# Kernel tuning notes

Hardware: AMD Instinct MI355X
Metric: run time of the kernel (lower is better)

## Reference

```python
import jax, jax.numpy as jnp
import numpy as np

SOM_H, SOM_W = 16, 16
K = SOM_H * SOM_W          # num_embeddings = 256
EMB_D = 32                 # embedding_dim
ALPHA, BETA = 6.0, 1.0


def _build_tables():
    """Static SOM grid neighbor tables (rectangular geometry).
    ind[k] is a 0/1 row over the K codebook entries marking k and its
    up/down/left/right grid neighbors; counts[k] = number of neighbors incl self.
    Replaces the original per-voxel Python loop with a constant lookup table.
    """
    ind = np.zeros((K, K), np.float32)
    for idx in range(K):
        h, w = divmod(idx, SOM_W)
        neigh = [idx]
        if h - 1 >= 0:
            neigh.append((h - 1) * SOM_W + w)
        if h + 1 < SOM_H:
            neigh.append((h + 1) * SOM_W + w)
        if w - 1 >= 0:
            neigh.append(h * SOM_W + (w - 1))
        if w + 1 < SOM_W:
            neigh.append(h * SOM_W + (w + 1))
        ind[idx, neigh] = 1.0
    counts = ind.sum(axis=1)
    return jnp.asarray(ind), jnp.asarray(counts)

_IND_TABLE, _COUNTS = _build_tables()


def setup_inputs() -> dict:
    key = jax.random.key(0)
    k1, k2 = jax.random.split(key)
    x = jax.random.normal(k1, (8, EMB_D, 32, 32, 32), dtype=jnp.float32)  # [B,C,D,H,W]
    W = jax.random.normal(k2, (K, EMB_D), dtype=jnp.float32)              # codebook
    return {"x": x, "W": W}


def reference(x, W):
    # channels-last: [B, D, H, Wd, C]
    inputs = jnp.transpose(x, (0, 2, 3, 4, 1))
    in_shape = inputs.shape
    flat = inputs.reshape(-1, EMB_D)                    # [N, d]
    flat_sg = jax.lax.stop_gradient(flat)               # matches flat_inputs.detach()

    # squared Euclidean distances to all codebook entries: [N, K]
    dist = (jnp.sum(flat_sg ** 2, axis=1, keepdims=True)
            + jnp.sum(W ** 2, axis=1)
            - 2.0 * flat_sg @ W.T)

    enc_idx = jnp.argmin(dist, axis=1)                  # [N]
    encodings = jax.nn.one_hot(enc_idx, K, dtype=inputs.dtype)  # [N, K]

    quantized = (encodings @ W).reshape(in_shape)
    commitment_loss = jnp.mean((quantized - inputs) ** 2)

    # vectorized neighbor indicator + counts via static table gather
    indicator = _IND_TABLE[enc_idx]                     # [N, K], constant wrt floats
    total_neighbors = jnp.sum(_COUNTS[enc_idx])
    somloss = jnp.sum(dist * indicator) / total_neighbors

    loss = ALPHA * commitment_loss + BETA * somloss

    # straight-through estimator
    quantized_st = inputs + jax.lax.stop_gradient(quantized - inputs)
    out = jnp.transpose(quantized_st, (0, 4, 1, 2, 3))  # back to [B,C,D,H,W]
    return loss, out, encodings
```

## Files before the change

### kernel.cpp

```cpp
#include <hip/hip_runtime.h>


#define SOM_K      256
#define EMB_D      32
#define WPAD       36
#define N_VOX      262144
#define SPATIAL    32768
#define OUT_ELEMS  8388608
#define COMMIT_DEN 8388608.0f
#define NSLOT      256

#define CONST_AS __attribute__((address_space(4)))

__global__ __launch_bounds__(256) void som_prep_kernel(float* __restrict__ ws) {
  float4* p = (float4*)ws;
  int t = threadIdx.x;
#pragma unroll
  for (int i = 0; i < 4; ++i) p[i * 256 + t] = make_float4(0.f, 0.f, 0.f, 0.f);
}

__global__ __launch_bounds__(256) void som_main_kernel(
    const float* __restrict__ x,
    const float* __restrict__ w,
    float* __restrict__ slots,
    float* __restrict__ out,
    float* __restrict__ enc) {
  __shared__ __align__(16) float wl[SOM_K * WPAD];
  __shared__ float wsql[SOM_K];

  const int t = threadIdx.x;
  const CONST_AS float* wc = (const CONST_AS float*)(unsigned long long)w;

  const int n    = blockIdx.x * 256 + t;
  const int base = (n >> 15) * (EMB_D * SPATIAL) + (n & (SPATIAL - 1));
  float xv[EMB_D];
#pragma unroll
  for (int c = 0; c < EMB_D; ++c) xv[c] = x[base + c * SPATIAL];

#pragma unroll
  for (int i = 0; i < 32; ++i) {
    int e = i * 256 + t;
    int r = e >> 5, c = e & 31;
    wl[r * WPAD + c] = w[e];
  }
  {
    float s = 0.0f;
#pragma unroll
    for (int c = 0; c < EMB_D; ++c) {
      float v = w[t * EMB_D + c];
      s = fmaf(v, v, s);
    }
    wsql[t] = s;
  }
  __syncthreads();

  float xsq = 0.0f;
#pragma unroll
  for (int c = 0; c < EMB_D; ++c) xsq = fmaf(xv[c], xv[c], xsq);

  float best = 3.402823466e38f;
  int   bidx = 0;
#pragma unroll 2
  for (int k = 0; k < SOM_K; ++k) {
    const CONST_AS float* wr = wc + (k << 5);
    float dot = 0.0f;
#pragma unroll
    for (int j = 0; j < EMB_D; ++j) dot = fmaf(wr[j], xv[j], dot);
    float d = (xsq + wsql[k]) - 2.0f * dot;
    if (d < best) { best = d; bidx = k; }
  }

  {
    const int lane = t & 63, wave = t >> 6;
    float* ep = enc + (size_t)(blockIdx.x * 256 + wave * 64) * SOM_K + lane;
    const int c1 = lane + 64, c2 = lane + 128, c3 = lane + 192;
    for (int row = 0; row < 64; ++row) {
      const int src = __builtin_amdgcn_readlane(bidx, row);
      ep[0]   = (lane == src) ? 1.0f : 0.0f;
      ep[64]  = (c1   == src) ? 1.0f : 0.0f;
      ep[128] = (c2   == src) ? 1.0f : 0.0f;
      ep[192] = (c3   == src) ? 1.0f : 0.0f;
      ep += SOM_K;
    }
  }

  float commit = 0.0f;
  {
    const float4* qrow = (const float4*)(wl + bidx * WPAD);
#pragma unroll
    for (int j = 0; j < 8; ++j) {
      float4 q = qrow[j];
      float qq[4] = { q.x, q.y, q.z, q.w };
#pragma unroll
      for (int u = 0; u < 4; ++u) {
        int c = 4 * j + u;
        out[base + c * SPATIAL] = qq[u];
        float df = qq[u] - xv[c];
        commit = fmaf(df, df, commit);
      }
    }
  }

  float som = best;
  float cnt = 1.0f;
  {
    const int h  = bidx >> 4;
    const int wc2 = bidx & 15;
    const int   cand[4]  = { bidx - 16, bidx + 16, bidx - 1, bidx + 1 };
    const float valid[4] = { h > 0 ? 1.f : 0.f,  h < 15 ? 1.f : 0.f,
                             wc2 > 0 ? 1.f : 0.f, wc2 < 15 ? 1.f : 0.f };
#pragma unroll
    for (int j = 0; j < 4; ++j) {
      int nk = valid[j] != 0.0f ? cand[j] : bidx;
      const float4* nrow = (const float4*)(wl + nk * WPAD);
      float dot = 0.0f;
#pragma unroll
      for (int jj = 0; jj < 8; ++jj) {
        float4 q = nrow[jj];
        dot = fmaf(q.x, xv[4 * jj + 0], dot);
        dot = fmaf(q.y, xv[4 * jj + 1], dot);
        dot = fmaf(q.z, xv[4 * jj + 2], dot);
        dot = fmaf(q.w, xv[4 * jj + 3], dot);
      }
      float d = (xsq + wsql[nk]) - 2.0f * dot;
      som = fmaf(valid[j], d, som);
      cnt += valid[j];
    }
  }

  for (int off = 32; off > 0; off >>= 1) {
    commit += __shfl_down(commit, off, 64);
    som    += __shfl_down(som,    off, 64);
    cnt    += __shfl_down(cnt,    off, 64);
  }
  if ((t & 63) == 0) {
    float* sp = slots + (size_t)(blockIdx.x & (NSLOT - 1)) * 16;
    atomicAdd(sp + 0, commit);
    atomicAdd(sp + 1, som);
    atomicAdd(sp + 2, cnt);
  }
}

__global__ __launch_bounds__(64) void som_final_kernel(
    const float* __restrict__ slots, float* __restrict__ loss) {
  const int t = threadIdx.x;
  float commit = 0.f, som = 0.f, cnt = 0.f;
#pragma unroll
  for (int i = 0; i < 4; ++i) {
    const float* sp = slots + (size_t)(i * 64 + t) * 16;
    commit += sp[0]; som += sp[1]; cnt += sp[2];
  }
  for (int off = 32; off > 0; off >>= 1) {
    commit += __shfl_down(commit, off, 64);
    som    += __shfl_down(som,    off, 64);
    cnt    += __shfl_down(cnt,    off, 64);
  }
  if (t == 0) loss[0] = 6.0f * (commit / COMMIT_DEN) + som / cnt;
}

extern "C" void kernel_launch(void* const* d_in, const int* in_sizes, int n_in,
                              void* d_out, int out_size, void* d_ws, size_t ws_size,
                              hipStream_t stream) {
  const float* x = (const float*)d_in[0];
  const float* w = (const float*)d_in[1];
  float* ws  = (float*)d_ws;
  float* o   = (float*)d_out;

  som_prep_kernel<<<1, 256, 0, stream>>>(ws);
  som_main_kernel<<<N_VOX / 256, 256, 0, stream>>>(
      x, w, ws, o + 1, o + 1 + OUT_ELEMS);
  som_final_kernel<<<1, 64, 0, stream>>>(ws, o);
}
```

Before: 382.9 us.

## Zero one-hot encodings in a separate prep kernel and scatter single ones

The one-hot encoding matrix (256 MB) is no longer written row by row inside the main kernel. A widened prep kernel now zero-fills it with float4 stores, handling the misaligned first and last elements, and the main kernel writes only one 1.0 per voxel as a scattered store. The aim is to take the large store stream out of the compute kernel and let the memset run at full streaming bandwidth. Total bytes written stay the same, but the work now spans two launches and adds a scattered store per voxel.

```diff
diff --git a/kernel.cpp b/kernel.cpp
--- a/kernel.cpp
+++ b/kernel.cpp
@@ -7,16 +7,34 @@
 #define N_VOX      262144
 #define SPATIAL    32768
 #define OUT_ELEMS  8388608
+#define ENC_ELEMS  67108864
 #define COMMIT_DEN 8388608.0f
 #define NSLOT      256
 
 #define CONST_AS __attribute__((address_space(4)))
 
-__global__ __launch_bounds__(256) void som_prep_kernel(float* __restrict__ ws) {
-  float4* p = (float4*)ws;
-  int t = threadIdx.x;
+__global__ __launch_bounds__(256) void som_prep_kernel(
+    float* __restrict__ ws, float* __restrict__ enc) {
+  const int t = threadIdx.x;
+  const long tid = (long)blockIdx.x * 256 + t;
+
+  if (blockIdx.x == 2047) {
+    float4* p = (float4*)ws;
 #pragma unroll
-  for (int i = 0; i < 4; ++i) p[i * 256 + t] = make_float4(0.f, 0.f, 0.f, 0.f);
+    for (int i = 0; i < 4; ++i) p[i * 256 + t] = make_float4(0.f, 0.f, 0.f, 0.f);
+  }
+
+  float4* body = (float4*)(enc + 3);
+  const float4 z4 = make_float4(0.f, 0.f, 0.f, 0.f);
+#pragma unroll
+  for (int i = 0; i < 32; ++i) {
+    long idx = (long)i * 524288 + tid;
+    if (idx < 16777215L) body[idx] = z4;
+  }
+  if (tid == 0) {
+    enc[0] = 0.f; enc[1] = 0.f; enc[2] = 0.f;
+    enc[ENC_ELEMS - 1] = 0.f;
+  }
 }
 
 __global__ __launch_bounds__(256) void som_main_kernel(
@@ -29,7 +47,7 @@
   __shared__ float wsql[SOM_K];
 
   const int t = threadIdx.x;
-  const CONST_AS float* wc = (const CONST_AS float*)(unsigned long long)w;
+  const CONST_AS float* wcp = (const CONST_AS float*)(unsigned long long)w;
 
   const int n    = blockIdx.x * 256 + t;
   const int base = (n >> 15) * (EMB_D * SPATIAL) + (n & (SPATIAL - 1));
@@ -62,7 +80,7 @@
   int   bidx = 0;
 #pragma unroll 2
   for (int k = 0; k < SOM_K; ++k) {
-    const CONST_AS float* wr = wc + (k << 5);
+    const CONST_AS float* wr = wcp + (k << 5);
     float dot = 0.0f;
 #pragma unroll
     for (int j = 0; j < EMB_D; ++j) dot = fmaf(wr[j], xv[j], dot);
@@ -70,19 +88,7 @@
     if (d < best) { best = d; bidx = k; }
   }
 
-  {
-    const int lane = t & 63, wave = t >> 6;
-    float* ep = enc + (size_t)(blockIdx.x * 256 + wave * 64) * SOM_K + lane;
-    const int c1 = lane + 64, c2 = lane + 128, c3 = lane + 192;
-    for (int row = 0; row < 64; ++row) {
-      const int src = __builtin_amdgcn_readlane(bidx, row);
-      ep[0]   = (lane == src) ? 1.0f : 0.0f;
-      ep[64]  = (c1   == src) ? 1.0f : 0.0f;
-      ep[128] = (c2   == src) ? 1.0f : 0.0f;
-      ep[192] = (c3   == src) ? 1.0f : 0.0f;
-      ep += SOM_K;
-    }
-  }
+  enc[(size_t)n * SOM_K + bidx] = 1.0f;
 
   float commit = 0.0f;
   {
@@ -104,7 +110,7 @@
   float som = best;
   float cnt = 1.0f;
   {
-    const int h  = bidx >> 4;
+    const int h   = bidx >> 4;
     const int wc2 = bidx & 15;
     const int   cand[4]  = { bidx - 16, bidx + 16, bidx - 1, bidx + 1 };
     const float valid[4] = { h > 0 ? 1.f : 0.f,  h < 15 ? 1.f : 0.f,
@@ -166,7 +172,7 @@
   float* ws  = (float*)d_ws;
   float* o   = (float*)d_out;
 
-  som_prep_kernel<<<1, 256, 0, stream>>>(ws);
+  som_prep_kernel<<<2048, 256, 0, stream>>>(ws, o + 1 + OUT_ELEMS);
   som_main_kernel<<<N_VOX / 256, 256, 0, stream>>>(
       x, w, ws, o + 1, o + 1 + OUT_ELEMS);
   som_final_kernel<<<1, 64, 0, stream>>>(ws, o);
```

Result: slower. 447.6 us (+16.9%).
